# Kernel optimization log

Measured on AMD Instinct MI355X. Metric: run time of the kernel, lower is better.

Reference implementation:

```python
import jax, jax.numpy as jnp
import numpy as np

GROUP_SIZE = 128
TOKENS, IN_F, OUT_F = 8192, 3072, 8192


def dequantize_weights(packed_int4, scales, group_size):
    # packed_int4: int32 [out, in//2] with values in [0,256) (uint8 semantics)
    # scales: float32 [out, in//group_size]
    out_f, half = packed_int4.shape
    in_f = half * 2
    w_even = packed_int4 & 15          # low nibble -> even columns
    w_odd = (packed_int4 >> 4) & 15    # high nibble -> odd columns
    w_even = jnp.where(w_even >= 8, w_even - 16, w_even)
    w_odd = jnp.where(w_odd >= 8, w_odd - 16, w_odd)
    # interleave even/odd along last axis -> [out, in]
    w_int = jnp.stack([w_even, w_odd], axis=-1).reshape(out_f, in_f)
    w_f = w_int.astype(jnp.float32).reshape(out_f, in_f // group_size, group_size)
    w_hat = w_f * scales[:, :, None]
    return w_hat.reshape(out_f, in_f)


def setup_inputs() -> dict:
    key = jax.random.key(0)
    k1, k2, k3, k4 = jax.random.split(key, 4)
    x = jax.random.normal(k1, (TOKENS, IN_F), dtype=jnp.float32)
    packed_int4 = jax.random.randint(k2, (OUT_F, IN_F // 2), 0, 256, dtype=jnp.int32)
    # positive per-group scales, typical magnitude for abs_max/7 of unit-scale weights
    scales = jax.random.uniform(k3, (OUT_F, IN_F // GROUP_SIZE), dtype=jnp.float32) * 0.01 + 1e-4
    bias = jax.random.normal(k4, (OUT_F,), dtype=jnp.float32) * 0.01
    return {"x": x, "packed_int4": packed_int4, "scales": scales, "bias": bias}


def reference(x, packed_int4, scales, bias):
    w_hat = dequantize_weights(packed_int4, scales, GROUP_SIZE)  # [out, in]
    # F.linear: y = x @ W^T + b
    return jnp.matmul(x, w_hat.T) + bias
```

## Files before the change

kernel.cpp:

```cpp
#include <hip/hip_runtime.h>
#include <stdint.h>

#define TOKENS 8192
#define IN_F   3072
#define OUT_F  8192
#define GROUP  128

#define BM 128
#define BN 128
#define BK 32

typedef __bf16 bf16x8 __attribute__((ext_vector_type(8)));
typedef float  f32x4  __attribute__((ext_vector_type(4)));

__device__ __forceinline__ uint32_t f2bf(float f) {
    union { float f; uint32_t u; } v; v.f = f;
    uint32_t u = v.u;
    return (u + 0x7fffu + ((u >> 16) & 1u)) >> 16;
}

__device__ __forceinline__ void async_cp16(const uint16_t* g, uint16_t* l) {
    __builtin_amdgcn_global_load_lds(
        (const __attribute__((address_space(1))) void*)g,
        (__attribute__((address_space(3))) void*)l,
        16, 0, 0);
}

__global__ __launch_bounds__(256) void dequant_w(const int* __restrict__ packed,
                                                 const float* __restrict__ scales,
                                                 uint16_t* __restrict__ W) {
    const int t   = blockIdx.x * 256 + threadIdx.x;
    const int idx = t * 4;
    const int row  = idx / (IN_F / 2);
    const int pcol = idx - row * (IN_F / 2);
    const int grp  = pcol >> 6;
    const float s  = scales[row * (IN_F / GROUP) + grp];

    const int4 p = *(const int4*)(packed + idx);
    int vals[4] = {p.x, p.y, p.z, p.w};
    uint32_t w[4];
#pragma unroll
    for (int i = 0; i < 4; ++i) {
        int b  = vals[i] & 255;
        int lo = b & 15;        lo = (lo >= 8) ? lo - 16 : lo;
        int hi = (b >> 4) & 15; hi = (hi >= 8) ? hi - 16 : hi;
        uint32_t e = f2bf((float)lo * s);
        uint32_t o = f2bf((float)hi * s);
        w[i] = e | (o << 16);
    }
    uint4 res = {w[0], w[1], w[2], w[3]};
    *(uint4*)(W + (size_t)idx * 2) = res;
}

__global__ __launch_bounds__(256) void cvt_x(const float* __restrict__ x,
                                             uint16_t* __restrict__ xb) {
    const size_t idx = ((size_t)blockIdx.x * 256 + threadIdx.x) * 8;
    const float4 a = *(const float4*)(x + idx);
    const float4 b = *(const float4*)(x + idx + 4);
    uint32_t w0 = f2bf(a.x) | (f2bf(a.y) << 16);
    uint32_t w1 = f2bf(a.z) | (f2bf(a.w) << 16);
    uint32_t w2 = f2bf(b.x) | (f2bf(b.y) << 16);
    uint32_t w3 = f2bf(b.z) | (f2bf(b.w) << 16);
    uint4 res = {w0, w1, w2, w3};
    *(uint4*)(xb + idx) = res;
}

__global__ __launch_bounds__(256, 2) void gemm_bt(const uint16_t* __restrict__ A,
                                                  const uint16_t* __restrict__ B,
                                                  const float* __restrict__ bias,
                                                  float* __restrict__ C) {
    constexpr int K = IN_F;
    constexpr int N = OUT_F;

    __shared__ __align__(16) uint16_t sA[BM * BK];
    __shared__ __align__(16) uint16_t sB[BN * BK];

    const int t    = threadIdx.x;
    const int bx   = blockIdx.x;
    const int by   = blockIdx.y;
    const int lane = t & 63;
    const int wave = t >> 6;
    const int wm   = (wave >> 1) * 64;
    const int wn   = (wave & 1) * 64;

    const int arow = t >> 2;
    const int acol = (t & 3) * 8;
    const uint16_t* gA = A + (size_t)(by * BM + arow) * K + acol;
    const uint16_t* gB = B + (size_t)(bx * BN + arow) * K + acol;
    uint16_t* lA = sA + t * 8;
    uint16_t* lB = sB + t * 8;

    const int fr = lane & 15;
    const int fk = (lane >> 4) * 8;

    f32x4 acc[4][4] = {};

    for (int k0 = 0; k0 < K; k0 += BK) {
        async_cp16(gA + k0,              lA);
        async_cp16(gA + k0 + 64 * K,     lA + 64 * BK);
        async_cp16(gB + k0,              lB);
        async_cp16(gB + k0 + 64 * K,     lB + 64 * BK);
        __syncthreads();

        bf16x8 af[4], bf[4];
#pragma unroll
        for (int i = 0; i < 4; ++i)
            af[i] = *(const bf16x8*)(sA + (wm + i * 16 + fr) * BK + fk);
#pragma unroll
        for (int j = 0; j < 4; ++j)
            bf[j] = *(const bf16x8*)(sB + (wn + j * 16 + fr) * BK + fk);

#pragma unroll
        for (int i = 0; i < 4; ++i)
#pragma unroll
            for (int j = 0; j < 4; ++j)
                acc[i][j] = __builtin_amdgcn_mfma_f32_16x16x32_bf16(af[i], bf[j], acc[i][j], 0, 0, 0);

        __syncthreads();
    }

    const int cr = (lane >> 4) * 4;
    const int cc = lane & 15;
#pragma unroll
    for (int j = 0; j < 4; ++j) {
        const int col = bx * BN + wn + j * 16 + cc;
        const float bv = bias[col];
#pragma unroll
        for (int i = 0; i < 4; ++i) {
            const size_t base = (size_t)(by * BM + wm + i * 16 + cr) * N + col;
#pragma unroll
            for (int r = 0; r < 4; ++r)
                C[base + (size_t)r * N] = acc[i][j][r] + bv;
        }
    }
}

extern "C" void kernel_launch(void* const* d_in, const int* in_sizes, int n_in,
                              void* d_out, int out_size, void* d_ws, size_t ws_size,
                              hipStream_t stream) {
    const float* x      = (const float*)d_in[0];
    const int*   packed = (const int*)d_in[1];
    const float* scales = (const float*)d_in[2];
    const float* bias   = (const float*)d_in[3];
    float*       out    = (float*)d_out;

    uint16_t* W  = (uint16_t*)d_ws;
    uint16_t* Xb = (uint16_t*)((char*)d_ws + (size_t)OUT_F * IN_F * 2);

    const int dq_blocks  = (OUT_F * (IN_F / 2) / 4) / 256;
    const int cvt_blocks = (TOKENS * IN_F / 8) / 256;

    dequant_w<<<dq_blocks, 256, 0, stream>>>(packed, scales, W);
    cvt_x<<<cvt_blocks, 256, 0, stream>>>(x, Xb);

    dim3 grid(OUT_F / BN, TOKENS / BM);
    gemm_bt<<<grid, 256, 0, stream>>>(Xb, W, bias, out);
}
```

Measured before the change: 849.6 us.

## Enlarge GEMM tile to 128x256x64 with XOR-swizzled LDS layout

```diff
diff --git a/kernel.cpp b/kernel.cpp
--- a/kernel.cpp
+++ b/kernel.cpp
@@ -7,8 +7,8 @@
 #define GROUP  128
 
 #define BM 128
-#define BN 128
-#define BK 32
+#define BN 256
+#define BK 64
 
 typedef __bf16 bf16x8 __attribute__((ext_vector_type(8)));
 typedef float  f32x4  __attribute__((ext_vector_type(4)));
@@ -65,10 +65,10 @@
     *(uint4*)(xb + idx) = res;
 }
 
-__global__ __launch_bounds__(256, 2) void gemm_bt(const uint16_t* __restrict__ A,
-                                                  const uint16_t* __restrict__ B,
-                                                  const float* __restrict__ bias,
-                                                  float* __restrict__ C) {
+__global__ __launch_bounds__(256) void gemm_bt(const uint16_t* __restrict__ A,
+                                               const uint16_t* __restrict__ B,
+                                               const float* __restrict__ bias,
+                                               float* __restrict__ C) {
     constexpr int K = IN_F;
     constexpr int N = OUT_F;
 
@@ -76,53 +76,59 @@
     __shared__ __align__(16) uint16_t sB[BN * BK];
 
     const int t    = threadIdx.x;
+    const int lane = t & 63;
+    const int wave = t >> 6;
     const int bx   = blockIdx.x;
     const int by   = blockIdx.y;
-    const int lane = t & 63;
-    const int wave = t >> 6;
     const int wm   = (wave >> 1) * 64;
-    const int wn   = (wave & 1) * 64;
+    const int wn   = (wave & 1) * 128;
 
-    const int arow = t >> 2;
-    const int acol = (t & 3) * 8;
-    const uint16_t* gA = A + (size_t)(by * BM + arow) * K + acol;
-    const uint16_t* gB = B + (size_t)(bx * BN + arow) * K + acol;
+    const int srow = t >> 3;
+    const int gch  = (t & 7) ^ (srow & 7);
+    const uint16_t* gA = A + (size_t)(by * BM + srow) * K + gch * 8;
+    const uint16_t* gB = B + (size_t)(bx * BN + srow) * K + gch * 8;
     uint16_t* lA = sA + t * 8;
     uint16_t* lB = sB + t * 8;
 
     const int fr = lane & 15;
-    const int fk = (lane >> 4) * 8;
+    const int qq = lane >> 4;
 
-    f32x4 acc[4][4] = {};
+    f32x4 acc[4][8] = {};
 
     for (int k0 = 0; k0 < K; k0 += BK) {
-        async_cp16(gA + k0,              lA);
-        async_cp16(gA + k0 + 64 * K,     lA + 64 * BK);
-        async_cp16(gB + k0,              lB);
-        async_cp16(gB + k0 + 64 * K,     lB + 64 * BK);
+#pragma unroll
+        for (int p = 0; p < 4; ++p)
+            async_cp16(gA + k0 + (size_t)(32 * p) * K, lA + 2048 * p);
+#pragma unroll
+        for (int p = 0; p < 8; ++p)
+            async_cp16(gB + k0 + (size_t)(32 * p) * K, lB + 2048 * p);
         __syncthreads();
 
-        bf16x8 af[4], bf[4];
 #pragma unroll
-        for (int i = 0; i < 4; ++i)
-            af[i] = *(const bf16x8*)(sA + (wm + i * 16 + fr) * BK + fk);
+        for (int ks = 0; ks < 2; ++ks) {
+            const int q = ks * 4 + qq;
+            bf16x8 af[4];
 #pragma unroll
-        for (int j = 0; j < 4; ++j)
-            bf[j] = *(const bf16x8*)(sB + (wn + j * 16 + fr) * BK + fk);
-
+            for (int i = 0; i < 4; ++i) {
+                const int row = wm + i * 16 + fr;
+                af[i] = *(const bf16x8*)(sA + row * 64 + (q ^ (row & 7)) * 8);
+            }
 #pragma unroll
-        for (int i = 0; i < 4; ++i)
+            for (int j = 0; j < 8; ++j) {
+                const int row = wn + j * 16 + fr;
+                const bf16x8 bf = *(const bf16x8*)(sB + row * 64 + (q ^ (row & 7)) * 8);
 #pragma unroll
-            for (int j = 0; j < 4; ++j)
-                acc[i][j] = __builtin_amdgcn_mfma_f32_16x16x32_bf16(af[i], bf[j], acc[i][j], 0, 0, 0);
-
+                for (int i = 0; i < 4; ++i)
+                    acc[i][j] = __builtin_amdgcn_mfma_f32_16x16x32_bf16(af[i], bf, acc[i][j], 0, 0, 0);
+            }
+        }
         __syncthreads();
     }
 
     const int cr = (lane >> 4) * 4;
     const int cc = lane & 15;
 #pragma unroll
-    for (int j = 0; j < 4; ++j) {
+    for (int j = 0; j < 8; ++j) {
         const int col = bx * BN + wn + j * 16 + cc;
         const float bv = bias[col];
 #pragma unroll
```

Result: slower. 1.014 ms (+19.3%).
